# Performance work log

Hardware: AMD Instinct MI355X
Metric: run time of the kernel (lower is better)

The kernel has to match this reference:

```python
import jax, jax.numpy as jnp
import numpy as np

N_NODES = 100000
K_NEIGH = 16
C = 128
B = 1


def setup_inputs() -> dict:
    key = jax.random.key(0)
    k1, k2, k3, k4, k5, k6 = jax.random.split(key, 6)
    inp = jax.random.normal(k1, (B, C, N_NODES), dtype=jnp.float32)
    adj = jax.random.randint(k2, (N_NODES, K_NEIGH), 0, N_NODES)
    w1 = jax.random.normal(k3, (C, C), dtype=jnp.float32) * 0.05
    b1 = jax.random.normal(k4, (C,), dtype=jnp.float32) * 0.05
    w2 = jax.random.normal(k5, (C, C), dtype=jnp.float32) * 0.05
    b2 = jax.random.normal(k6, (C,), dtype=jnp.float32) * 0.05
    return {"input": inp, "adj": adj, "w1": w1, "b1": b1, "w2": w2, "b2": b2}


def reference(input, adj, w1, b1, w2, b2):
    # fc1: 1x1 conv == channel-mixing matmul. input: [B, C, N]
    state_in = jnp.einsum('oc,bcn->bon', w1, input) + b1[None, :, None]
    # gather neighbor features: [B, C, N, K], mean over neighbors -> [B, C, N]
    neigh = input[:, :, adj]            # [B, C, N, K]
    agg = neigh.mean(axis=3)            # [B, C, N]
    fwd = jnp.einsum('oc,bcn->bon', w2, agg) + b2[None, :, None]
    return state_in + fwd
```

## Files before the change

kernel.cpp:

```cpp
#include <hip/hip_runtime.h>
#include <stdint.h>

#define N_NODES 100000
#define CH 128
#define K_NEIGH 16
#define TN 32
#define XT_STRIDE 36
#define XS_STRIDE 68
#define PS 132

#define PSWZ(n, o) ((n) * PS + ((o) ^ ((((n) >> 3) & 3) << 3)))


typedef short bf8v __attribute__((ext_vector_type(8)));
typedef float f32x4 __attribute__((ext_vector_type(4)));

__device__ __forceinline__ uint32_t pack_bf16x2(float a, float b) {
    union { float f; uint32_t u; } ua, ub;
    ua.f = a; ub.f = b;
    const uint32_t ra = (ua.u + 0x7fffu + ((ua.u >> 16) & 1u)) >> 16;
    const uint32_t rb = (ub.u + 0x7fffu + ((ub.u >> 16) & 1u)) >> 16;
    return ra | (rb << 16);
}
__device__ __forceinline__ uint16_t bf16_rne(float f) {
    union { float f; uint32_t u; } c; c.f = f;
    return (uint16_t)((c.u + 0x7fffu + ((c.u >> 16) & 1u)) >> 16);
}
__device__ __forceinline__ float bf16_tof(uint16_t h) {
    union { uint32_t u; float f; } c; c.u = ((uint32_t)h) << 16; return c.f;
}
__device__ __forceinline__ float bf16_lo(uint32_t u) {
    union { uint32_t u; float f; } c; c.u = u << 16; return c.f;
}
__device__ __forceinline__ float bf16_hi(uint32_t u) {
    union { uint32_t u; float f; } c; c.u = u & 0xffff0000u; return c.f;
}

__global__ void k_wcvt(const float* __restrict__ W,
                       uint16_t* __restrict__ Wh, uint16_t* __restrict__ Wl) {
    const int i = blockIdx.x * 256 + threadIdx.x;
    if (i < CH * CH) {
        const float f = W[i];
        const uint16_t h = bf16_rne(f);
        Wh[i] = h;
        Wl[i] = bf16_rne(f - bf16_tof(h));
    }
}

__global__ __launch_bounds__(256, 2) void k_w2x_mfma(
    const float*    __restrict__ X,
    const uint16_t* __restrict__ W2h,
    const uint16_t* __restrict__ W2l,
    uint16_t*       __restrict__ Yt)
{
    __shared__ __align__(16) uint16_t XsH[64 * 128];
    __shared__ __align__(16) uint16_t XsL[64 * 128];

    const int t  = threadIdx.x;
    const int n0 = blockIdx.x * 64;
    const int V  = (N_NODES - n0 < 64) ? (N_NODES - n0) : 64;

    for (int it = 0; it < 8; ++it) {
        const int idx = t + it * 256;
        const int nq = idx & 15, c = idx >> 4;
        float4 v = make_float4(0.f, 0.f, 0.f, 0.f);
        if (nq * 4 < V)
            v = *(const float4*)&X[(size_t)c * N_NODES + n0 + nq * 4];
        const float vv0 = v.x, vv1 = v.y, vv2 = v.z, vv3 = v.w;
#pragma unroll
        for (int s = 0; s < 4; ++s) {
            const float f = (s == 0) ? vv0 : (s == 1) ? vv1 : (s == 2) ? vv2 : vv3;
            const int n = nq * 4 + s;
            const uint16_t h = bf16_rne(f);
            const uint16_t lo = bf16_rne(f - bf16_tof(h));
            const int byi = (n << 8) + (((c * 2)) ^ ((n & 7) << 4));
            XsH[byi >> 1] = h;
            XsL[byi >> 1] = lo;
        }
    }

    const int l = t & 63;
    const int w = t >> 6;
    bf8v ah[2][4], al[2][4];
    const int ar = l & 15;
    const int ac = (l >> 4) * 8;
#pragma unroll
    for (int ot = 0; ot < 2; ++ot)
#pragma unroll
        for (int ks = 0; ks < 4; ++ks) {
            const size_t off = (size_t)(w * 32 + ot * 16 + ar) * CH + ks * 32 + ac;
            ah[ot][ks] = *(const bf8v*)&W2h[off];
            al[ot][ks] = *(const bf8v*)&W2l[off];
        }
    __syncthreads();

    f32x4 d[2][4];
#pragma unroll
    for (int ot = 0; ot < 2; ++ot)
#pragma unroll
        for (int nt = 0; nt < 4; ++nt)
            d[ot][nt] = (f32x4){0.f, 0.f, 0.f, 0.f};

#pragma unroll
    for (int ks = 0; ks < 4; ++ks) {
#pragma unroll
        for (int nt = 0; nt < 4; ++nt) {
            const int n  = nt * 16 + (l & 15);
            const int byi = (n << 8) + ((ks * 64 + ((l >> 4) * 16)) ^ ((n & 7) << 4));
            const bf8v bh = *(const bf8v*)((const char*)XsH + byi);
            const bf8v bl = *(const bf8v*)((const char*)XsL + byi);
#pragma unroll
            for (int ot = 0; ot < 2; ++ot) {
                d[ot][nt] = __builtin_amdgcn_mfma_f32_16x16x32_bf16(
                    ah[ot][ks], bh, d[ot][nt], 0, 0, 0);
                d[ot][nt] = __builtin_amdgcn_mfma_f32_16x16x32_bf16(
                    al[ot][ks], bh, d[ot][nt], 0, 0, 0);
                d[ot][nt] = __builtin_amdgcn_mfma_f32_16x16x32_bf16(
                    ah[ot][ks], bl, d[ot][nt], 0, 0, 0);
            }
        }
    }

#pragma unroll
    for (int ot = 0; ot < 2; ++ot)
#pragma unroll
        for (int nt = 0; nt < 4; ++nt) {
            const int n = nt * 16 + (l & 15);
            if (n < V) {
                const int o4 = w * 32 + ot * 16 + (l >> 4) * 4;
                uint2 pv;
                pv.x = pack_bf16x2(d[ot][nt][0], d[ot][nt][1]);
                pv.y = pack_bf16x2(d[ot][nt][2], d[ot][nt][3]);
                *(uint2*)&Yt[(size_t)(n0 + n) * CH + o4] = pv;
            }
        }
}

__global__ __launch_bounds__(256, 8) void k_main(
    const float*    __restrict__ X,
    const int*      __restrict__ adj,
    const float*    __restrict__ W1,
    const float*    __restrict__ B1,
    const float*    __restrict__ B2,
    const uint16_t* __restrict__ Yt,
    float*          __restrict__ Out)
{
    __shared__ __align__(16) float Xs[CH * XT_STRIDE];
    __shared__ __align__(16) int adjS[TN * K_NEIGH];

    const int t  = threadIdx.x;
    const int n0 = blockIdx.x * TN;

    if (t < 128)
        *(int4*)&adjS[t * 4] = *(const int4*)&adj[(size_t)n0 * K_NEIGH + t * 4];
    for (int it = 0; it < 4; ++it) {
        const int idx = t + it * 256;
        const int nq = idx & 7, c = idx >> 3;
        *(float4*)&Xs[c * XT_STRIDE + nq * 4] =
            *(const float4*)&X[(size_t)c * N_NODES + n0 + nq * 4];
    }
    __syncthreads();

    const int ng = t & 7, og = t >> 3;
    float acc[4][4];
#pragma unroll
    for (int i = 0; i < 4; ++i)
#pragma unroll
        for (int j = 0; j < 4; ++j) acc[i][j] = 0.0f;

    const float* wp = W1 + (size_t)(og * 4) * CH;
#pragma unroll 1
    for (int c0 = 0; c0 < CH; c0 += 4) {
        float4 wq[4];
#pragma unroll
        for (int i = 0; i < 4; ++i)
            wq[i] = *(const float4*)&wp[i * CH + c0];
#pragma unroll
        for (int e = 0; e < 4; ++e) {
            const float4 xv = *(const float4*)&Xs[(c0 + e) * XT_STRIDE + ng * 4];
#pragma unroll
            for (int i = 0; i < 4; ++i) {
                const float w = ((const float*)&wq[i])[e];
                acc[i][0] = fmaf(w, xv.x, acc[i][0]);
                acc[i][1] = fmaf(w, xv.y, acc[i][1]);
                acc[i][2] = fmaf(w, xv.z, acc[i][2]);
                acc[i][3] = fmaf(w, xv.w, acc[i][3]);
            }
        }
    }

    __syncthreads();
    float* P = Xs;
#pragma unroll
    for (int j = 0; j < 4; ++j) {
        const int n = ng * 4 + j;
        float4 v = make_float4(acc[0][j], acc[1][j], acc[2][j], acc[3][j]);
        *(float4*)&P[PSWZ(n, og * 4)] = v;
    }
    __syncthreads();

    {
        const int l4 = (t & 31) * 4;
        const int g  = t >> 5;
        for (int itp = 0; itp < 4; ++itp) {
            const int n = itp * 8 + g;
            int js[K_NEIGH];
#pragma unroll
            for (int k = 0; k < K_NEIGH; ++k) js[k] = adjS[n * K_NEIGH + k];
            float4 a0 = make_float4(0.f, 0.f, 0.f, 0.f);
            float4 a1 = make_float4(0.f, 0.f, 0.f, 0.f);
#pragma unroll
            for (int k = 0; k < K_NEIGH; k += 2) {
                const uint2 v0 = *(const uint2*)&Yt[(size_t)js[k]     * CH + l4];
                const uint2 v1 = *(const uint2*)&Yt[(size_t)js[k + 1] * CH + l4];
                a0.x += bf16_lo(v0.x); a0.y += bf16_hi(v0.x);
                a0.z += bf16_lo(v0.y); a0.w += bf16_hi(v0.y);
                a1.x += bf16_lo(v1.x); a1.y += bf16_hi(v1.x);
                a1.z += bf16_lo(v1.y); a1.w += bf16_hi(v1.y);
            }
            float4 cur = *(const float4*)&P[PSWZ(n, l4)];
            cur.x += (a0.x + a1.x) * 0.0625f;
            cur.y += (a0.y + a1.y) * 0.0625f;
            cur.z += (a0.z + a1.z) * 0.0625f;
            cur.w += (a0.w + a1.w) * 0.0625f;
            *(float4*)&P[PSWZ(n, l4)] = cur;
        }
    }
    __syncthreads();

    for (int it = 0; it < 4; ++it) {
        const int idx = t + it * 256;
        const int o = idx >> 3, nq = idx & 7;
        const float bb = B1[o] + B2[o];
        float4 v;
        v.x = P[PSWZ(nq * 4 + 0, o)] + bb;
        v.y = P[PSWZ(nq * 4 + 1, o)] + bb;
        v.z = P[PSWZ(nq * 4 + 2, o)] + bb;
        v.w = P[PSWZ(nq * 4 + 3, o)] + bb;
        *(float4*)&Out[(size_t)o * N_NODES + n0 + nq * 4] = v;
    }
}

__global__ __launch_bounds__(256, 2) void k_fused_legacy(
    const float* __restrict__ X,
    const int*   __restrict__ adj,
    const float* __restrict__ W1,
    const float* __restrict__ B1,
    const float* __restrict__ W2,
    const float* __restrict__ B2,
    float*       __restrict__ Out)
{
    __shared__ __align__(16) float Xs[CH * XS_STRIDE];
    __shared__ __align__(16) float As[CH * XS_STRIDE];
    __shared__ int adjS[64 * K_NEIGH];

    const int t  = threadIdx.x;
    const int n0 = blockIdx.x * 64;
    const int V  = (N_NODES - n0 < 64) ? (N_NODES - n0) : 64;

    {
        const int base  = n0 * K_NEIGH;
        const int valid = V * K_NEIGH;
        for (int idx = t; idx < 64 * K_NEIGH; idx += 256)
            adjS[idx] = (idx < valid) ? adj[base + idx] : 0;
    }
    for (int it = 0; it < 32; ++it) {
        const int idx = t + it * 256;
        const int n = idx & 63, c = idx >> 6;
        Xs[c * XS_STRIDE + n] =
            (n < V) ? X[(size_t)c * N_NODES + n0 + n] : 0.0f;
    }
    __syncthreads();

    {
        const int n_l = t & 63, q = t >> 6;
        int js[K_NEIGH];
#pragma unroll
        for (int k = 0; k < K_NEIGH; ++k) js[k] = adjS[n_l * K_NEIGH + k];
        if (n_l < V) {
            for (int cc = 0; cc < 32; ++cc) {
                const int c = q * 32 + cc;
                const float* xc = X + (size_t)c * N_NODES;
                float s = 0.0f;
#pragma unroll
                for (int k = 0; k < K_NEIGH; ++k) s += xc[js[k]];
                As[c * XS_STRIDE + n_l] = s * 0.0625f;
            }
        } else {
            for (int cc = 0; cc < 32; ++cc)
                As[(q * 32 + cc) * XS_STRIDE + n_l] = 0.0f;
        }
    }
    __syncthreads();

    const int ng = t & 7, og = t >> 3;
    float acc[4][8];
#pragma unroll
    for (int i = 0; i < 4; ++i)
#pragma unroll
        for (int j = 0; j < 8; ++j) acc[i][j] = 0.0f;

    const float* w1p = W1 + (og * 4) * CH;
    const float* w2p = W2 + (og * 4) * CH;
    for (int c = 0; c < CH; ++c) {
        float xv[8], av[8], w1v[4], w2v[4];
        *(float4*)&xv[0] = *(const float4*)&Xs[c * XS_STRIDE + ng * 8];
        *(float4*)&xv[4] = *(const float4*)&Xs[c * XS_STRIDE + ng * 8 + 4];
        *(float4*)&av[0] = *(const float4*)&As[c * XS_STRIDE + ng * 8];
        *(float4*)&av[4] = *(const float4*)&As[c * XS_STRIDE + ng * 8 + 4];
#pragma unroll
        for (int i = 0; i < 4; ++i) {
            w1v[i] = w1p[i * CH + c];
            w2v[i] = w2p[i * CH + c];
        }
#pragma unroll
        for (int i = 0; i < 4; ++i)
#pragma unroll
            for (int j = 0; j < 8; ++j)
                acc[i][j] += w1v[i] * xv[j] + w2v[i] * av[j];
    }

    __syncthreads();
    float* Zt = Xs;
#pragma unroll
    for (int i = 0; i < 4; ++i) {
        *(float4*)&Zt[(og * 4 + i) * XS_STRIDE + ng * 8]     = *(float4*)&acc[i][0];
        *(float4*)&Zt[(og * 4 + i) * XS_STRIDE + ng * 8 + 4] = *(float4*)&acc[i][4];
    }
    __syncthreads();
    for (int it = 0; it < 32; ++it) {
        const int idx = t + it * 256;
        const int n = idx & 63, o = idx >> 6;
        if (n < V) {
            Out[(size_t)o * N_NODES + n0 + n] =
                Zt[o * XS_STRIDE + n] + B1[o] + B2[o];
        }
    }
}

extern "C" void kernel_launch(void* const* d_in, const int* in_sizes, int n_in,
                              void* d_out, int out_size, void* d_ws, size_t ws_size,
                              hipStream_t stream) {
    const float* X   = (const float*)d_in[0];
    const int*   adj = (const int*)d_in[1];
    const float* W1  = (const float*)d_in[2];
    const float* B1  = (const float*)d_in[3];
    const float* W2  = (const float*)d_in[4];
    const float* B2  = (const float*)d_in[5];
    float* Out = (float*)d_out;

    const size_t yt_bytes = (size_t)N_NODES * CH * sizeof(uint16_t);
    const size_t w_bytes  = (size_t)CH * CH * sizeof(uint16_t);
    const size_t need     = yt_bytes + 2 * w_bytes;

    if (ws_size >= need) {
        uint16_t* Yt  = (uint16_t*)d_ws;
        uint16_t* W2h = Yt + (size_t)N_NODES * CH;
        uint16_t* W2l = W2h + (size_t)CH * CH;
        k_wcvt<<<(CH * CH + 255) / 256, 256, 0, stream>>>(W2, W2h, W2l);
        const int nb1 = (N_NODES + 63) / 64;
        k_w2x_mfma<<<nb1, 256, 0, stream>>>(X, W2h, W2l, Yt);
        const int nb2 = N_NODES / TN;
        k_main<<<nb2, 256, 0, stream>>>(X, adj, W1, B1, B2, Yt, Out);
    } else {
        const int nblocks = (N_NODES + 63) / 64;
        k_fused_legacy<<<nblocks, 256, 0, stream>>>(X, adj, W1, B1, W2, B2, Out);
    }
}
```

Before: 248.9 us.

## Move W1 matmul into MFMA kernel alongside W2, gather kernel accumulates into output

The W1 channel-mixing matmul moves out of the scalar FMA loop in the main kernel and into the bf16 split-precision MFMA kernel, which now computes W1·X and W2·X from the same staged X tile. That kernel writes state_in plus both biases straight to the output, and the gather kernel reads the output back and adds the neighbour mean. This removes the second read of X and the fp32 FMA work from the gather kernel. In exchange the output is written and then read-modify-written, and the first kernel holds twice as many accumulators, with strided uncoalesced output stores.

```diff
diff --git a/kernel.cpp b/kernel.cpp
--- a/kernel.cpp
+++ b/kernel.cpp
@@ -5,7 +5,6 @@
 #define CH 128
 #define K_NEIGH 16
 #define TN 32
-#define XT_STRIDE 36
 #define XS_STRIDE 68
 #define PS 132
 
@@ -47,11 +46,16 @@
     }
 }
 
-__global__ __launch_bounds__(256, 2) void k_w2x_mfma(
+__global__ __launch_bounds__(256, 2) void k_dual(
     const float*    __restrict__ X,
+    const uint16_t* __restrict__ W1h,
+    const uint16_t* __restrict__ W1l,
     const uint16_t* __restrict__ W2h,
     const uint16_t* __restrict__ W2l,
-    uint16_t*       __restrict__ Yt)
+    const float*    __restrict__ B1,
+    const float*    __restrict__ B2,
+    uint16_t*       __restrict__ Yt,
+    float*          __restrict__ Out)
 {
     __shared__ __align__(16) uint16_t XsH[64 * 128];
     __shared__ __align__(16) uint16_t XsL[64 * 128];
@@ -71,38 +75,39 @@
         for (int s = 0; s < 4; ++s) {
             const float f = (s == 0) ? vv0 : (s == 1) ? vv1 : (s == 2) ? vv2 : vv3;
             const int n = nq * 4 + s;
+            const int byi = (n << 8) + (((c * 2)) ^ ((n & 7) << 4));
             const uint16_t h = bf16_rne(f);
-            const uint16_t lo = bf16_rne(f - bf16_tof(h));
-            const int byi = (n << 8) + (((c * 2)) ^ ((n & 7) << 4));
             XsH[byi >> 1] = h;
-            XsL[byi >> 1] = lo;
-        }
-    }
+            XsL[byi >> 1] = bf16_rne(f - bf16_tof(h));
+        }
+    }
+    __syncthreads();
 
     const int l = t & 63;
     const int w = t >> 6;
-    bf8v ah[2][4], al[2][4];
     const int ar = l & 15;
     const int ac = (l >> 4) * 8;
+
+    f32x4 d1[2][4], d2[2][4];
 #pragma unroll
     for (int ot = 0; ot < 2; ++ot)
 #pragma unroll
-        for (int ks = 0; ks < 4; ++ks) {
+        for (int nt = 0; nt < 4; ++nt) {
+            d1[ot][nt] = (f32x4){0.f, 0.f, 0.f, 0.f};
+            d2[ot][nt] = (f32x4){0.f, 0.f, 0.f, 0.f};
+        }
+
+#pragma unroll
+    for (int ks = 0; ks < 4; ++ks) {
+        bf8v a1h[2], a1l[2], a2h[2], a2l[2];
+#pragma unroll
+        for (int ot = 0; ot < 2; ++ot) {
             const size_t off = (size_t)(w * 32 + ot * 16 + ar) * CH + ks * 32 + ac;
-            ah[ot][ks] = *(const bf8v*)&W2h[off];
-            al[ot][ks] = *(const bf8v*)&W2l[off];
-        }
-    __syncthreads();
-
-    f32x4 d[2][4];
-#pragma unroll
-    for (int ot = 0; ot < 2; ++ot)
-#pragma unroll
-        for (int nt = 0; nt < 4; ++nt)
-            d[ot][nt] = (f32x4){0.f, 0.f, 0.f, 0.f};
-
-#pragma unroll
-    for (int ks = 0; ks < 4; ++ks) {
+            a1h[ot] = *(const bf8v*)&W1h[off];
+            a1l[ot] = *(const bf8v*)&W1l[off];
+            a2h[ot] = *(const bf8v*)&W2h[off];
+            a2l[ot] = *(const bf8v*)&W2l[off];
+        }
 #pragma unroll
         for (int nt = 0; nt < 4; ++nt) {
             const int n  = nt * 16 + (l & 15);
@@ -111,12 +116,36 @@
             const bf8v bl = *(const bf8v*)((const char*)XsL + byi);
 #pragma unroll
             for (int ot = 0; ot < 2; ++ot) {
-                d[ot][nt] = __builtin_amdgcn_mfma_f32_16x16x32_bf16(
-                    ah[ot][ks], bh, d[ot][nt], 0, 0, 0);
-                d[ot][nt] = __builtin_amdgcn_mfma_f32_16x16x32_bf16(
-                    al[ot][ks], bh, d[ot][nt], 0, 0, 0);
-                d[ot][nt] = __builtin_amdgcn_mfma_f32_16x16x32_bf16(
-                    ah[ot][ks], bl, d[ot][nt], 0, 0, 0);
+                d1[ot][nt] = __builtin_amdgcn_mfma_f32_16x16x32_bf16(
+                    a1h[ot], bh, d1[ot][nt], 0, 0, 0);
+                d1[ot][nt] = __builtin_amdgcn_mfma_f32_16x16x32_bf16(
+                    a1l[ot], bh, d1[ot][nt], 0, 0, 0);
+                d1[ot][nt] = __builtin_amdgcn_mfma_f32_16x16x32_bf16(
+                    a1h[ot], bl, d1[ot][nt], 0, 0, 0);
+                d2[ot][nt] = __builtin_amdgcn_mfma_f32_16x16x32_bf16(
+                    a2h[ot], bh, d2[ot][nt], 0, 0, 0);
+                d2[ot][nt] = __builtin_amdgcn_mfma_f32_16x16x32_bf16(
+                    a2l[ot], bh, d2[ot][nt], 0, 0, 0);
+            }
+        }
+    }
+
+#pragma unroll
+    for (int ot = 0; ot < 2; ++ot) {
+        const int ob = w * 32 + ot * 16 + (l >> 4) * 4;
+        const float b0 = B1[ob + 0] + B2[ob + 0];
+        const float b1 = B1[ob + 1] + B2[ob + 1];
+        const float b2 = B1[ob + 2] + B2[ob + 2];
+        const float b3 = B1[ob + 3] + B2[ob + 3];
+#pragma unroll
+        for (int nt = 0; nt < 4; ++nt) {
+            const int n = nt * 16 + (l & 15);
+            if (n < V) {
+                float* op = Out + (size_t)ob * N_NODES + n0 + n;
+                op[0]                   = d1[ot][nt][0] + b0;
+                op[(size_t)N_NODES]     = d1[ot][nt][1] + b1;
+                op[(size_t)N_NODES * 2] = d1[ot][nt][2] + b2;
+                op[(size_t)N_NODES * 3] = d1[ot][nt][3] + b3;
             }
         }
     }
@@ -129,23 +158,19 @@
             if (n < V) {
                 const int o4 = w * 32 + ot * 16 + (l >> 4) * 4;
                 uint2 pv;
-                pv.x = pack_bf16x2(d[ot][nt][0], d[ot][nt][1]);
-                pv.y = pack_bf16x2(d[ot][nt][2], d[ot][nt][3]);
+                pv.x = pack_bf16x2(d2[ot][nt][0], d2[ot][nt][1]);
+                pv.y = pack_bf16x2(d2[ot][nt][2], d2[ot][nt][3]);
                 *(uint2*)&Yt[(size_t)(n0 + n) * CH + o4] = pv;
             }
         }
 }
 
-__global__ __launch_bounds__(256, 8) void k_main(
-    const float*    __restrict__ X,
+__global__ __launch_bounds__(256, 8) void k_gather(
     const int*      __restrict__ adj,
-    const float*    __restrict__ W1,
-    const float*    __restrict__ B1,
-    const float*    __restrict__ B2,
     const uint16_t* __restrict__ Yt,
     float*          __restrict__ Out)
 {
-    __shared__ __align__(16) float Xs[CH * XT_STRIDE];
+    __shared__ __align__(16) float P[TN * PS];
     __shared__ __align__(16) int adjS[TN * K_NEIGH];
 
     const int t  = threadIdx.x;
@@ -153,50 +178,6 @@
 
     if (t < 128)
         *(int4*)&adjS[t * 4] = *(const int4*)&adj[(size_t)n0 * K_NEIGH + t * 4];
-    for (int it = 0; it < 4; ++it) {
-        const int idx = t + it * 256;
-        const int nq = idx & 7, c = idx >> 3;
-        *(float4*)&Xs[c * XT_STRIDE + nq * 4] =
-            *(const float4*)&X[(size_t)c * N_NODES + n0 + nq * 4];
-    }
-    __syncthreads();
-
-    const int ng = t & 7, og = t >> 3;
-    float acc[4][4];
-#pragma unroll
-    for (int i = 0; i < 4; ++i)
-#pragma unroll
-        for (int j = 0; j < 4; ++j) acc[i][j] = 0.0f;
-
-    const float* wp = W1 + (size_t)(og * 4) * CH;
-#pragma unroll 1
-    for (int c0 = 0; c0 < CH; c0 += 4) {
-        float4 wq[4];
-#pragma unroll
-        for (int i = 0; i < 4; ++i)
-            wq[i] = *(const float4*)&wp[i * CH + c0];
-#pragma unroll
-        for (int e = 0; e < 4; ++e) {
-            const float4 xv = *(const float4*)&Xs[(c0 + e) * XT_STRIDE + ng * 4];
-#pragma unroll
-            for (int i = 0; i < 4; ++i) {
-                const float w = ((const float*)&wq[i])[e];
-                acc[i][0] = fmaf(w, xv.x, acc[i][0]);
-                acc[i][1] = fmaf(w, xv.y, acc[i][1]);
-                acc[i][2] = fmaf(w, xv.z, acc[i][2]);
-                acc[i][3] = fmaf(w, xv.w, acc[i][3]);
-            }
-        }
-    }
-
-    __syncthreads();
-    float* P = Xs;
-#pragma unroll
-    for (int j = 0; j < 4; ++j) {
-        const int n = ng * 4 + j;
-        float4 v = make_float4(acc[0][j], acc[1][j], acc[2][j], acc[3][j]);
-        *(float4*)&P[PSWZ(n, og * 4)] = v;
-    }
     __syncthreads();
 
     {
@@ -218,12 +199,12 @@
                 a1.x += bf16_lo(v1.x); a1.y += bf16_hi(v1.x);
                 a1.z += bf16_lo(v1.y); a1.w += bf16_hi(v1.y);
             }
-            float4 cur = *(const float4*)&P[PSWZ(n, l4)];
-            cur.x += (a0.x + a1.x) * 0.0625f;
-            cur.y += (a0.y + a1.y) * 0.0625f;
-            cur.z += (a0.z + a1.z) * 0.0625f;
-            cur.w += (a0.w + a1.w) * 0.0625f;
-            *(float4*)&P[PSWZ(n, l4)] = cur;
+            float4 s;
+            s.x = (a0.x + a1.x) * 0.0625f;
+            s.y = (a0.y + a1.y) * 0.0625f;
+            s.z = (a0.z + a1.z) * 0.0625f;
+            s.w = (a0.w + a1.w) * 0.0625f;
+            *(float4*)&P[PSWZ(n, l4)] = s;
         }
     }
     __syncthreads();
@@ -231,13 +212,13 @@
     for (int it = 0; it < 4; ++it) {
         const int idx = t + it * 256;
         const int o = idx >> 3, nq = idx & 7;
-        const float bb = B1[o] + B2[o];
-        float4 v;
-        v.x = P[PSWZ(nq * 4 + 0, o)] + bb;
-        v.y = P[PSWZ(nq * 4 + 1, o)] + bb;
-        v.z = P[PSWZ(nq * 4 + 2, o)] + bb;
-        v.w = P[PSWZ(nq * 4 + 3, o)] + bb;
-        *(float4*)&Out[(size_t)o * N_NODES + n0 + nq * 4] = v;
+        float* op = Out + (size_t)o * N_NODES + n0 + nq * 4;
+        float4 cur = *(const float4*)op;
+        cur.x += P[PSWZ(nq * 4 + 0, o)];
+        cur.y += P[PSWZ(nq * 4 + 1, o)];
+        cur.z += P[PSWZ(nq * 4 + 2, o)];
+        cur.w += P[PSWZ(nq * 4 + 3, o)];
+        *(float4*)op = cur;
     }
 }
 
@@ -349,19 +330,23 @@
     const float* B2  = (const float*)d_in[5];
     float* Out = (float*)d_out;
 
-    const size_t yt_bytes = (size_t)N_NODES * CH * sizeof(uint16_t);
-    const size_t w_bytes  = (size_t)CH * CH * sizeof(uint16_t);
-    const size_t need     = yt_bytes + 2 * w_bytes;
+    const size_t yt_elems = (size_t)N_NODES * CH;
+    const size_t w_elems  = (size_t)CH * CH;
+    const size_t need = (yt_elems + 4 * w_elems) * sizeof(uint16_t);
 
     if (ws_size >= need) {
         uint16_t* Yt  = (uint16_t*)d_ws;
-        uint16_t* W2h = Yt + (size_t)N_NODES * CH;
-        uint16_t* W2l = W2h + (size_t)CH * CH;
-        k_wcvt<<<(CH * CH + 255) / 256, 256, 0, stream>>>(W2, W2h, W2l);
+        uint16_t* W1h = Yt + yt_elems;
+        uint16_t* W1l = W1h + w_elems;
+        uint16_t* W2h = W1l + w_elems;
+        uint16_t* W2l = W2h + w_elems;
+        const int wcb = (CH * CH + 255) / 256;
+        k_wcvt<<<wcb, 256, 0, stream>>>(W1, W1h, W1l);
+        k_wcvt<<<wcb, 256, 0, stream>>>(W2, W2h, W2l);
         const int nb1 = (N_NODES + 63) / 64;
-        k_w2x_mfma<<<nb1, 256, 0, stream>>>(X, W2h, W2l, Yt);
+        k_dual<<<nb1, 256, 0, stream>>>(X, W1h, W1l, W2h, W2l, B1, B2, Yt, Out);
         const int nb2 = N_NODES / TN;
-        k_main<<<nb2, 256, 0, stream>>>(X, adj, W1, B1, B2, Yt, Out);
+        k_gather<<<nb2, 256, 0, stream>>>(adj, Yt, Out);
     } else {
         const int nblocks = (N_NODES + 63) / 64;
         k_fused_legacy<<<nblocks, 256, 0, stream>>>(X, adj, W1, B1, W2, B2, Out);
```

New measurement: 236.8 us. 4.9% less time.
